# Performance work log

Hardware: AMD Instinct MI355X
Metric: run time of the kernel (lower is better)

## Reference

```python
import jax, jax.numpy as jnp
import numpy as np

RADIUS = 5
KS = 2 * RADIUS + 1  # 11
SIGMA_X2 = 4.0 ** 2  # 16
SIGMA_I2 = 10.0 ** 2  # 100


def _patches(x):
    """x: [N,1,H,W] -> [N, H*W, KS, KS] zero-padded sliding windows (torch Unfold semantics)."""
    N, _, H, W = x.shape
    p = jax.lax.conv_general_dilated_patches(
        x, (KS, KS), (1, 1), [(RADIUS, RADIUS), (RADIUS, RADIUS)]
    )  # [N, KS*KS, H, W], channel dim ordered (kh, kw)
    return p.reshape(N, KS, KS, H * W).transpose(0, 3, 1, 2)


def _distance_map(dtype):
    d = (jnp.arange(KS, dtype=dtype) - RADIUS) ** 2
    return jnp.exp(-(d[:, None] + d[None, :]) / SIGMA_X2)  # [KS, KS]


def setup_inputs() -> dict:
    key = jax.random.key(0)
    k1, k2 = jax.random.split(key)
    images = jax.random.uniform(k1, (8, 1, 224, 224), dtype=jnp.float32)
    labels = jax.random.uniform(k2, (8, 4, 224, 224), dtype=jnp.float32)
    return {"images": images, "labels": labels}


def reference(images, labels):
    B, _, H, W = images.shape
    K = labels.shape[1]
    HW = H * W

    img = images * 255.0
    regions = _patches(img)                                   # [B,HW,KS,KS]
    mask = _patches(jnp.ones((1, 1, H, W), img.dtype))        # [1,HW,KS,KS], 0 on padding
    dist_map = _distance_map(img.dtype)                       # [KS,KS]

    i_f = img.reshape(B, HW)[:, :, None, None]                # center pixel intensity
    weights = dist_map * jnp.exp(-(regions - i_f) ** 2 / SIGMA_I2) * mask  # [B,HW,KS,KS]

    # class-prob patches for all classes at once
    P = _patches(labels.reshape(B * K, 1, H, W)).reshape(B, K, HW, KS, KS)

    num = jnp.einsum('bnij,bknij->bkn', weights, P)           # sum_j w_ij * p_j
    den = weights.sum(axis=(2, 3))                            # [B,HW], sum_j w_ij
    p_f = labels.reshape(B, K, HW)

    ratio = jnp.einsum('bkn,bkn->bk', p_f, num) / jnp.einsum('bkn,bn->bk', p_f, den)
    # per-class L1Loss(ratio, 0) = mean over batch of |ratio|; summed over classes
    ratio_sum = jnp.abs(ratio).mean(axis=0).sum()
    return K - ratio_sum
```

## Files before the change

kernel.cpp:

```cpp
#include <hip/hip_runtime.h>
#include <type_traits>

typedef float f2 __attribute__((ext_vector_type(2)));
typedef float f4 __attribute__((ext_vector_type(4)));
typedef _Float16 h2t __attribute__((ext_vector_type(2)));

constexpr int Hh = 224, Ww = 224, Bb = 8, Kc = 4, RAD = 5;

constexpr int TX = 32;
constexpr int TILEH = 32;
constexpr int NTHR = 512;
constexpr int SW = TX + 2 * RAD;
constexpr int SH = TILEH + 2 * RAD;
constexpr int SSTR = SW + 1;
constexpr int GXD = Ww / TX;
constexpr int GYD = Hh / TILEH;
constexpr int PB = GXD * GYD;

constexpr float LOG2E = 1.44269504f;
constexpr float KI = -0.01f * LOG2E;
constexpr float DSC = -0.0625f * LOG2E;
constexpr float D2[12] = {25.f,16.f,9.f,4.f,1.f,0.f,1.f,4.f,9.f,16.f,25.f,1e5f};

static __device__ inline f4 splat4(float x) { return (f4){x, x, x, x}; }

static __device__ inline float pack2(float a, float b) {
    return __builtin_bit_cast(float, __builtin_amdgcn_cvt_pkrtz(a, b));
}
static __device__ inline f4 unpack4(float y, float z) {
    const h2t a = __builtin_bit_cast(h2t, y);
    const h2t b = __builtin_bit_cast(h2t, z);
    return (f4){(float)a.x, (float)a.y, (float)b.x, (float)b.y};
}

__global__ __launch_bounds__(NTHR, 4) void ncut_main(const float* __restrict__ images,
                                                     const float* __restrict__ labels,
                                                     float* __restrict__ acc) {
    __shared__ f4 stap[SH * SSTR];
    __shared__ float red[8][8];

    const int b   = blockIdx.z;
    const int x0  = blockIdx.x * TX;
    const int y0  = blockIdx.y * TILEH;
    const int tid = threadIdx.x;

    const float* imgb = images + (size_t)b * (Hh * Ww);
    const float* labb = labels + (size_t)b * (Kc * Hh * Ww);

    for (int idx = tid; idx < SH * SSTR; idx += NTHR) {
        const int lx = idx % SSTR, ly = idx / SSTR;
        const int gx = x0 - RAD + lx, gy = y0 - RAD + ly;
        float iv = 1e19f, p01 = 0.f, p23 = 0.f;
        if (lx < SW && gx >= 0 && gx < Ww && gy >= 0 && gy < Hh) {
            const int g = gy * Ww + gx;
            iv  = imgb[g] * 255.0f;
            p01 = pack2(labb[g], labb[Hh * Ww + g]);
            p23 = pack2(labb[2 * Hh * Ww + g], labb[3 * Hh * Ww + g]);
        }
        stap[idx] = (f4){iv, p01, p23, 0.f};
    }
    __syncthreads();

    const int tx  = tid & 31;
    const int ty  = (tid >> 5) & 7;
    const int grp = tid >> 8;
    const int r0  = 4 * ty;

    f4 crec[4];
    float c[4];
#pragma unroll
    for (int p = 0; p < 4; ++p) {
        crec[p] = stap[(r0 + p + RAD) * SSTR + tx + RAD];
        c[p] = crec[p].x;
    }

    f4 num[4];
    f2 den[4];
#pragma unroll
    for (int p = 0; p < 4; ++p) { num[p] = splat4(0.f); den[p] = (f2){0.f, 0.f}; }

    auto body = [&](auto GC) {
        constexpr int G = decltype(GC)::value;
#pragma unroll
        for (int d = 0; d < 7; ++d) {
            const int dr = 7 * G + d;
            const int rowoff = (r0 + dr) * SSTR + tx;
#pragma unroll
            for (int i = 0; i < 6; ++i) {
                const f4 rA = stap[rowoff + 2 * i];
                const f4 rB = stap[rowoff + 2 * i + 1];
                const f2 v  = (f2){rA.x, rB.x};
                const f4 a0 = unpack4(rA.y, rA.z);
                const f4 a1 = unpack4(rB.y, rB.z);
#pragma unroll
                for (int p = 0; p < 4; ++p) {
                    if (dr >= p && dr <= p + 10) {
                        const f2 base = (f2){(D2[2 * i] + D2[dr - p]) * DSC,
                                             (D2[2 * i + 1] + D2[dr - p]) * DSC};
                        const f2 dd = v - c[p];
                        const f2 a = __builtin_elementwise_fma(dd * KI, dd, base);
                        const float e0 = __builtin_amdgcn_exp2f(a.x);
                        const float e1 = __builtin_amdgcn_exp2f(a.y);
                        den[p] += (f2){e0, e1};
                        num[p] = __builtin_elementwise_fma(splat4(e0), a0, num[p]);
                        num[p] = __builtin_elementwise_fma(splat4(e1), a1, num[p]);
                    }
                }
            }
        }
    };
    if (grp == 0) body(std::integral_constant<int, 0>{});
    else          body(std::integral_constant<int, 1>{});

    f4 numv = splat4(0.f), denv = splat4(0.f);
#pragma unroll
    for (int p = 0; p < 4; ++p) {
        const f4 pc = unpack4(crec[p].y, crec[p].z);
        const float dn = den[p].x + den[p].y;
        numv = __builtin_elementwise_fma(pc, num[p], numv);
        denv = __builtin_elementwise_fma(pc, splat4(dn), denv);
    }

    float vals[8] = {numv.x, numv.y, numv.z, numv.w, denv.x, denv.y, denv.z, denv.w};

#pragma unroll
    for (int i = 0; i < 8; ++i) {
        float v = vals[i];
#pragma unroll
        for (int off = 32; off > 0; off >>= 1) v += __shfl_down(v, off, 64);
        vals[i] = v;
    }

    const int wave = tid >> 6, lane = tid & 63;
    if (lane == 0) {
#pragma unroll
        for (int i = 0; i < 8; ++i) red[wave][i] = vals[i];
    }
    __syncthreads();

    if (tid < 8) {
        const int gid = blockIdx.x + GXD * blockIdx.y + GXD * GYD * blockIdx.z;
        float s = 0.f;
#pragma unroll
        for (int w = 0; w < 8; ++w) s += red[w][tid];
        acc[gid * 8 + tid] = s;
    }
}

__global__ void ncut_final(const float* __restrict__ acc, float* __restrict__ out) {
    __shared__ float red[4][64];
    const int t = threadIdx.x;
    const int combo = t & 63;
    const int chunk = t >> 6;
    const int k = combo & 3, b = (combo >> 2) & 7;
    const int part = combo >> 5;
    float s = 0.f;
    for (int j = chunk; j < PB; j += 4)
        s += acc[(b * PB + j) * 8 + k + 4 * part];
    red[chunk][combo] = s;
    __syncthreads();
    if (t < 64) {
        float v = red[0][t] + red[1][t] + red[2][t] + red[3][t];
        const float den = __shfl(v, (t + 32) & 63, 64);
        float r = (t < 32) ? fabsf(v / den) : 0.f;
#pragma unroll
        for (int off = 32; off > 0; off >>= 1) r += __shfl_down(r, off, 64);
        if (t == 0) out[0] = (float)Kc - r * (1.0f / (float)Bb);
    }
}

extern "C" void kernel_launch(void* const* d_in, const int* in_sizes, int n_in,
                              void* d_out, int out_size, void* d_ws, size_t ws_size,
                              hipStream_t stream) {
    const float* images = (const float*)d_in[0];
    const float* labels = (const float*)d_in[1];
    float* out = (float*)d_out;
    float* acc = (float*)d_ws;

    dim3 grid(GXD, GYD, Bb);
    ncut_main<<<grid, NTHR, 0, stream>>>(images, labels, acc);
    ncut_final<<<1, 256, 0, stream>>>(acc, out);
}
```

Baseline: 85.67 us.

## Exploit pairwise weight symmetry to evaluate only half of each window

The pairwise weight w_ij is symmetric, so each pixel now evaluates only forward neighbours: rows below it, plus the columns to its right in its own row. The numerator and denominator are rebuilt from these half-sums together with the unit self-weight. This roughly halves the exp2 and FMA work, and the shared tile only needs a halo below the block. Tiles are also shrunk to 32x16 with 256 threads, giving twice as many blocks at lower occupancy bounds, and per-thread bookkeeping changes from four centre rows to two.

Result: faster. 83.49 us, median of 2 (-2.5%).

```diff
diff --git a/kernel.cpp b/kernel.cpp
--- a/kernel.cpp
+++ b/kernel.cpp
@@ -1,5 +1,4 @@
 #include <hip/hip_runtime.h>
-#include <type_traits>
 
 typedef float f2 __attribute__((ext_vector_type(2)));
 typedef float f4 __attribute__((ext_vector_type(4)));
@@ -8,10 +7,10 @@
 constexpr int Hh = 224, Ww = 224, Bb = 8, Kc = 4, RAD = 5;
 
 constexpr int TX = 32;
-constexpr int TILEH = 32;
-constexpr int NTHR = 512;
+constexpr int TILEH = 16;
+constexpr int NTHR = 256;
 constexpr int SW = TX + 2 * RAD;
-constexpr int SH = TILEH + 2 * RAD;
+constexpr int SH = TILEH + RAD;
 constexpr int SSTR = SW + 1;
 constexpr int GXD = Ww / TX;
 constexpr int GYD = Hh / TILEH;
@@ -21,6 +20,7 @@
 constexpr float KI = -0.01f * LOG2E;
 constexpr float DSC = -0.0625f * LOG2E;
 constexpr float D2[12] = {25.f,16.f,9.f,4.f,1.f,0.f,1.f,4.f,9.f,16.f,25.f,1e5f};
+constexpr float DR2[6] = {0.f,1.f,4.f,9.f,16.f,25.f};
 
 static __device__ inline f4 splat4(float x) { return (f4){x, x, x, x}; }
 
@@ -33,11 +33,11 @@
     return (f4){(float)a.x, (float)a.y, (float)b.x, (float)b.y};
 }
 
-__global__ __launch_bounds__(NTHR, 4) void ncut_main(const float* __restrict__ images,
+__global__ __launch_bounds__(NTHR, 3) void ncut_main(const float* __restrict__ images,
                                                      const float* __restrict__ labels,
                                                      float* __restrict__ acc) {
     __shared__ f4 stap[SH * SSTR];
-    __shared__ float red[8][8];
+    __shared__ float red[4][8];
 
     const int b   = blockIdx.z;
     const int x0  = blockIdx.x * TX;
@@ -49,9 +49,9 @@
 
     for (int idx = tid; idx < SH * SSTR; idx += NTHR) {
         const int lx = idx % SSTR, ly = idx / SSTR;
-        const int gx = x0 - RAD + lx, gy = y0 - RAD + ly;
+        const int gx = x0 - RAD + lx, gy = y0 + ly;
         float iv = 1e19f, p01 = 0.f, p23 = 0.f;
-        if (lx < SW && gx >= 0 && gx < Ww && gy >= 0 && gy < Hh) {
+        if (lx < SW && gx >= 0 && gx < Ww && gy < Hh) {
             const int g = gy * Ww + gx;
             iv  = imgb[g] * 255.0f;
             p01 = pack2(labb[g], labb[Hh * Ww + g]);
@@ -61,74 +61,73 @@
     }
     __syncthreads();
 
-    const int tx  = tid & 31;
-    const int ty  = (tid >> 5) & 7;
-    const int grp = tid >> 8;
-    const int r0  = 4 * ty;
+    const int tx = tid & 31;
+    const int ty = tid >> 5;
+    const int r0 = 2 * ty;
 
-    f4 crec[4];
-    float c[4];
+    const f4 crec0 = stap[r0 * SSTR + tx + RAD];
+    const f4 crec1 = stap[(r0 + 1) * SSTR + tx + RAD];
+    const float c0 = crec0.x;
+    const float c1 = crec1.x;
+
+    f4 s1a = splat4(0.f), s1b = splat4(0.f);
+    f2 s0a = (f2){0.f, 0.f}, s0b = (f2){0.f, 0.f};
+
 #pragma unroll
-    for (int p = 0; p < 4; ++p) {
-        crec[p] = stap[(r0 + p + RAD) * SSTR + tx + RAD];
-        c[p] = crec[p].x;
-    }
-
-    f4 num[4];
-    f2 den[4];
+    for (int dr = 0; dr < 7; ++dr) {
+        const int rowoff = (r0 + dr) * SSTR + tx;
 #pragma unroll
-    for (int p = 0; p < 4; ++p) { num[p] = splat4(0.f); den[p] = (f2){0.f, 0.f}; }
-
-    auto body = [&](auto GC) {
-        constexpr int G = decltype(GC)::value;
-#pragma unroll
-        for (int d = 0; d < 7; ++d) {
-            const int dr = 7 * G + d;
-            const int rowoff = (r0 + dr) * SSTR + tx;
-#pragma unroll
-            for (int i = 0; i < 6; ++i) {
+        for (int i = 0; i < 6; ++i) {
+            const bool act0 = (dr <= 5) && (dr >= 1 || i >= 3);
+            const bool act1 = (dr >= 1) && (dr >= 2 || i >= 3);
+            if (act0 || act1) {
                 const f4 rA = stap[rowoff + 2 * i];
                 const f4 rB = stap[rowoff + 2 * i + 1];
                 const f2 v  = (f2){rA.x, rB.x};
-                const f4 a0 = unpack4(rA.y, rA.z);
-                const f4 a1 = unpack4(rB.y, rB.z);
-#pragma unroll
-                for (int p = 0; p < 4; ++p) {
-                    if (dr >= p && dr <= p + 10) {
-                        const f2 base = (f2){(D2[2 * i] + D2[dr - p]) * DSC,
-                                             (D2[2 * i + 1] + D2[dr - p]) * DSC};
-                        const f2 dd = v - c[p];
-                        const f2 a = __builtin_elementwise_fma(dd * KI, dd, base);
-                        const float e0 = __builtin_amdgcn_exp2f(a.x);
-                        const float e1 = __builtin_amdgcn_exp2f(a.y);
-                        den[p] += (f2){e0, e1};
-                        num[p] = __builtin_elementwise_fma(splat4(e0), a0, num[p]);
-                        num[p] = __builtin_elementwise_fma(splat4(e1), a1, num[p]);
-                    }
+                const f4 pa = unpack4(rA.y, rA.z);
+                const f4 pb = unpack4(rB.y, rB.z);
+                if (act0) {
+                    const f2 base = (f2){(D2[2 * i] + DR2[dr]) * DSC,
+                                         (D2[2 * i + 1] + DR2[dr]) * DSC};
+                    const f2 dd = v - c0;
+                    const f2 a = __builtin_elementwise_fma(dd * KI, dd, base);
+                    const float e0 = __builtin_amdgcn_exp2f(a.x);
+                    const float e1 = __builtin_amdgcn_exp2f(a.y);
+                    s0a += (f2){e0, e1};
+                    s1a = __builtin_elementwise_fma(splat4(e0), pa, s1a);
+                    s1a = __builtin_elementwise_fma(splat4(e1), pb, s1a);
+                }
+                if (act1) {
+                    const f2 base = (f2){(D2[2 * i] + DR2[dr - 1]) * DSC,
+                                         (D2[2 * i + 1] + DR2[dr - 1]) * DSC};
+                    const f2 dd = v - c1;
+                    const f2 a = __builtin_elementwise_fma(dd * KI, dd, base);
+                    const float e0 = __builtin_amdgcn_exp2f(a.x);
+                    const float e1 = __builtin_amdgcn_exp2f(a.y);
+                    s0b += (f2){e0, e1};
+                    s1b = __builtin_elementwise_fma(splat4(e0), pa, s1b);
+                    s1b = __builtin_elementwise_fma(splat4(e1), pb, s1b);
                 }
             }
         }
-    };
-    if (grp == 0) body(std::integral_constant<int, 0>{});
-    else          body(std::integral_constant<int, 1>{});
+    }
 
-    f4 numv = splat4(0.f), denv = splat4(0.f);
-#pragma unroll
-    for (int p = 0; p < 4; ++p) {
-        const f4 pc = unpack4(crec[p].y, crec[p].z);
-        const float dn = den[p].x + den[p].y;
-        numv = __builtin_elementwise_fma(pc, num[p], numv);
-        denv = __builtin_elementwise_fma(pc, splat4(dn), denv);
-    }
+    const f4 p0 = unpack4(crec0.y, crec0.z);
+    const f4 p1 = unpack4(crec1.y, crec1.z);
+    const float S0a = s0a.x + s0a.y;
+    const float S0b = s0b.x + s0b.y;
+
+    const f4 numv = p0 * (splat4(2.f) * s1a + p0) + p1 * (splat4(2.f) * s1b + p1);
+    const f4 denv = p0 * splat4(S0a + 1.f) + s1a + p1 * splat4(S0b + 1.f) + s1b;
 
     float vals[8] = {numv.x, numv.y, numv.z, numv.w, denv.x, denv.y, denv.z, denv.w};
 
 #pragma unroll
     for (int i = 0; i < 8; ++i) {
-        float v = vals[i];
+        float vv = vals[i];
 #pragma unroll
-        for (int off = 32; off > 0; off >>= 1) v += __shfl_down(v, off, 64);
-        vals[i] = v;
+        for (int off = 32; off > 0; off >>= 1) vv += __shfl_down(vv, off, 64);
+        vals[i] = vv;
     }
 
     const int wave = tid >> 6, lane = tid & 63;
@@ -140,10 +139,7 @@
 
     if (tid < 8) {
         const int gid = blockIdx.x + GXD * blockIdx.y + GXD * GYD * blockIdx.z;
-        float s = 0.f;
-#pragma unroll
-        for (int w = 0; w < 8; ++w) s += red[w][tid];
-        acc[gid * 8 + tid] = s;
+        acc[gid * 8 + tid] = red[0][tid] + red[1][tid] + red[2][tid] + red[3][tid];
     }
 }
 
```
